# Performance work log

Hardware: AMD Instinct MI355X
Metric: run time of the kernel (lower is better)

The kernel has to match this reference:

```python
import jax, jax.numpy as jnp
import numpy as np

E = 65536          # number of edges (cell pairs)
D = 256            # hidden_dim
P = 8              # n_lr_pairs


def setup_inputs() -> dict:
    key = jax.random.key(0)
    k1, k2, k3, k4, k5, k6, k7 = jax.random.split(key, 7)
    scale = 1.0 / np.sqrt(D)
    z_src = jax.random.normal(k1, (E, D), dtype=jnp.float32)
    z_dst = jax.random.normal(k2, (E, D), dtype=jnp.float32)
    lr_pair_idx = jax.random.randint(k3, (E,), 0, P, dtype=jnp.int64)
    # Per-LR-pair Linear(D, D): y = x @ W.T + b  (torch convention, W: [out, in])
    W_lr = jax.random.normal(k4, (P, D, D), dtype=jnp.float32) * scale
    b_lr = jax.random.normal(k5, (P, D), dtype=jnp.float32) * scale
    # nn.Bilinear(D, D, 1): weight [1, D, D], bias [1]
    W_bil = jax.random.normal(k6, (1, D, D), dtype=jnp.float32) * scale
    b_bil = jax.random.normal(k7, (1,), dtype=jnp.float32) * scale
    return {"z_src": z_src, "z_dst": z_dst, "W_lr": W_lr, "b_lr": b_lr,
            "W_bil": W_bil, "b_bil": b_bil, "lr_pair_idx": lr_pair_idx}


def _forward(z_src, z_dst, W_lr, b_lr, W_bil, b_bil, lr_pair_idx):
    # Per-LR-pair linear projection of z_src (MoE-style routing).
    # Fixed small loop over P experts; each iteration is a dense GEMM over
    # all E edges, masked to the edges routed to that pair. All idx values
    # lie in [0, P), so the zeros-init in the original is fully overwritten.
    z_proj = jnp.zeros_like(z_src)
    for p in range(P):
        mask = (lr_pair_idx == p)[:, None]                      # [E, 1]
        y_p = z_src @ W_lr[p].T + b_lr[p]                       # [E, D]
        z_proj = jnp.where(mask, y_p, z_proj)
    # Bilinear scoring: score_e = z_proj_e @ W_bil[0] @ z_dst_e + b_bil
    t = z_proj @ W_bil[0]                                       # [E, D]
    scores = jnp.sum(t * z_dst, axis=-1, keepdims=True) + b_bil  # [E, 1]
    return scores


def reference(z_src, z_dst, W_lr, b_lr, W_bil, b_bil, lr_pair_idx):
    return _forward(z_src, z_dst, W_lr, b_lr, W_bil, b_bil, lr_pair_idx)
```

## Files before the change

### kernel.cpp

```cpp
#include <hip/hip_runtime.h>
#include <hip/hip_bf16.h>
#include <cstddef>

#define NE 65536
#define ND 256
#define NP 8
#define RBLK 64
#define EPB (NE / RBLK)
#define TR 32
#define MAXT 2056

typedef short bf16x8 __attribute__((ext_vector_type(8)));
typedef float f32x4  __attribute__((ext_vector_type(4)));

__device__ __forceinline__ unsigned short f2bf(float f) {
  unsigned int u = __float_as_uint(f);
  u += 0x7FFFu + ((u >> 16) & 1u);
  return (unsigned short)(u >> 16);
}
__device__ __forceinline__ float bf2f(unsigned short h) {
  return __uint_as_float(((unsigned int)h) << 16);
}
__device__ __forceinline__ int load_idx(const void* idxraw, int is32, int e) {
  return is32 ? ((const int*)idxraw)[e] : (int)((const long long*)idxraw)[e];
}
__device__ __forceinline__ int sniff_is32(const void* idxraw, int* lflag, int bsel) {
  int tid = threadIdx.x;
  if (tid == 0) *lflag = 0;
  __syncthreads();
  const unsigned int* w = (const unsigned int*)idxraw;
  unsigned int val = w[((bsel & 63) * 256 + tid) * 2 + 1];
  if (__any(val != 0) && (tid & 63) == 0) atomicOr(lflag, 1);
  __syncthreads();
  return *lflag;
}

__global__ __launch_bounds__(256) void k_pre0(const float* __restrict__ Wbil,
                                              const float* __restrict__ blr,
                                              const void* __restrict__ idxraw,
                                              unsigned short* __restrict__ WbT,
                                              float* __restrict__ v,
                                              int* __restrict__ counts) {
  int b = blockIdx.x, t = threadIdx.x;
  if (b < 32) {
    int s = b * 256 + t;
    int kt = s >> 10, c = (s >> 6) & 15, l = s & 63;
    int col = c * 16 + (l & 15);
    int k0 = kt * 32 + (l >> 4) * 8;
    union { uint4 u; unsigned short h[8]; } uu;
#pragma unroll
    for (int j = 0; j < 8; ++j)
      uu.h[j] = f2bf(Wbil[(k0 + j) * ND + col]);
    *(uint4*)(WbT + (size_t)s * 8) = uu.u;
  } else if (b < 40) {
    int p = b - 32;
    float s = 0.f;
    for (int k = 0; k < ND; ++k)
      s = fmaf(blr[p * ND + k], Wbil[k * ND + t], s);
    v[p * ND + t] = s;
  } else {
    __shared__ int h[NP];
    __shared__ int lflag;
    int hb = b - 40;
    int is32 = sniff_is32(idxraw, &lflag, hb);
    if (t < NP) h[t] = 0;
    __syncthreads();
    int base = hb * EPB;
#pragma unroll
    for (int i = 0; i < EPB / 256; ++i) {
      int p = load_idx(idxraw, is32, base + t + i * 256);
      atomicAdd(&h[p], 1);
    }
    __syncthreads();
    if (t < NP) counts[hb * NP + t] = h[t];
  }
}

__global__ __launch_bounds__(64) void k_scan(const int* __restrict__ counts,
                                             int* __restrict__ hdr,
                                             int* __restrict__ bases) {
  __shared__ int cnt[NP];
  __shared__ int off[NP + 1];
  int q = threadIdx.x;
  if (q < NP) {
    int s = 0;
    for (int b = 0; b < RBLK; ++b) s += counts[b * NP + q];
    cnt[q] = s;
  }
  __syncthreads();
  if (q == 0) {
    int o = 0, tt = 0;
    for (int p = 0; p < NP; ++p) {
      off[p] = o; hdr[p] = o; hdr[9 + p] = tt;
      o += cnt[p];
      tt += (cnt[p] + TR - 1) / TR;
    }
    off[NP] = o; hdr[NP] = o; hdr[9 + NP] = tt;
  }
  __syncthreads();
  if (q < NP) {
    int run = off[q];
    for (int b = 0; b < RBLK; ++b) {
      bases[b * NP + q] = run;
      run += counts[b * NP + q];
    }
  }
}

__global__ __launch_bounds__(256) void k_sc2(const void* __restrict__ idxraw,
                                             const int* __restrict__ bases,
                                             int* __restrict__ perm,
                                             const float* __restrict__ Wlr,
                                             const unsigned short* __restrict__ WbT,
                                             unsigned short* __restrict__ Cst) {
  __shared__ unsigned short aF[2048 * 8];
  int b = blockIdx.x, tid = threadIdx.x;
  if (b < 64) {
    __shared__ int cur[NP];
    __shared__ int lflag;
    int is32 = sniff_is32(idxraw, &lflag, b);
    if (tid < NP) cur[tid] = bases[b * NP + tid];
    __syncthreads();
    int base = b * EPB;
#pragma unroll
    for (int i = 0; i < EPB / 256; ++i) {
      int e = base + tid + i * 256;
      int p = load_idx(idxraw, is32, e);
      int slot = atomicAdd(&cur[p], 1);
      perm[slot] = e;
    }
    return;
  }
  int blk = b - 64;
  int p = blk >> 2;
  int i0 = (blk & 3) * 64;
  const float* Wp = Wlr + (size_t)p * ND * ND;
#pragma unroll
  for (int it = 0; it < 8; ++it) {
    int s = tid + it * 256;
    int kt = s >> 8, r = (s >> 6) & 3, l = s & 63;
    int i = r * 16 + (l & 15);
    int k0 = kt * 32 + (l >> 4) * 8;
    union { uint4 u; unsigned short h[8]; } uu;
#pragma unroll
    for (int j = 0; j < 8; ++j)
      uu.h[j] = f2bf(Wp[(size_t)(k0 + j) * ND + i0 + i]);
    *(uint4*)(aF + (size_t)s * 8) = uu.u;
  }
  __syncthreads();
  int w = tid >> 6, l = tid & 63;
  f32x4 zero = {0.f, 0.f, 0.f, 0.f};
  f32x4 acc[16];
#pragma unroll
  for (int c = 0; c < 16; ++c) acc[c] = zero;
  for (int kt = 0; kt < 8; ++kt) {
    bf16x8 a = *(const bf16x8*)(aF + (size_t)((kt * 4 + w) * 64 + l) * 8);
#pragma unroll
    for (int c = 0; c < 16; ++c) {
      bf16x8 bb = *(const bf16x8*)(WbT + (size_t)((kt * 16 + c) * 64 + l) * 8);
      acc[c] = __builtin_amdgcn_mfma_f32_16x16x32_bf16(a, bb, acc[c], 0, 0, 0);
    }
  }
  unsigned short* Cp = Cst + (size_t)p * ND * ND;
#pragma unroll
  for (int c = 0; c < 16; ++c) {
#pragma unroll
    for (int q = 0; q < 4; ++q) {
      int i = i0 + w * 16 + ((l >> 4) * 4) + q;
      int j = c * 16 + (l & 15);
      int pos = ((i >> 5) * 16 + (j >> 4)) * 512 + (((i >> 3) & 3) * 16 + (j & 15)) * 8 + (i & 7);
      Cp[pos] = f2bf(acc[c][q]);
    }
  }
}

__global__ __launch_bounds__(512, 6) void k_main(const float* __restrict__ zsrc,
                                                 const float* __restrict__ zdst,
                                                 const int* __restrict__ perm,
                                                 const int* __restrict__ hdr,
                                                 const unsigned short* __restrict__ Cst,
                                                 const float* __restrict__ v,
                                                 const float* __restrict__ bbil,
                                                 float* __restrict__ out) {
  __shared__ unsigned short zs[8192];
  __shared__ unsigned short zd[8192];
  __shared__ float red[8][TR];
  int tid = threadIdx.x;
  int bid = blockIdx.x;
  if (bid >= hdr[9 + NP]) return;
  int p = 0;
#pragma unroll
  for (int q = 1; q < NP; ++q) p += (bid >= hdr[9 + q]) ? 1 : 0;
  int t = bid - hdr[9 + p];
  int cbeg = hdr[p], cend = hdr[p + 1];
  int ebase = cbeg + t * TR;
  int nrow = cend - ebase; if (nrow > TR) nrow = TR;
  int w = tid >> 6, l = tid & 63;

  int e4[4];
#pragma unroll
  for (int i = 0; i < 4; ++i) {
    int r = ebase + w * 4 + i; if (r > cend - 1) r = cend - 1;
    e4[i] = perm[r];
  }
  float4 fs[4], fd[4];
#pragma unroll
  for (int i = 0; i < 4; ++i)
    fs[i] = *(const float4*)(zsrc + (size_t)e4[i] * ND + l * 4);
#pragma unroll
  for (int i = 0; i < 4; ++i)
    fd[i] = *(const float4*)(zdst + (size_t)e4[i] * ND + l * 4);
  int kt0 = l >> 3, q0 = (l >> 1) & 3, par0 = l & 1;
#pragma unroll
  for (int i = 0; i < 4; ++i) {
    int row = w * 4 + i;
    union { unsigned long long u; unsigned short h[4]; } us, ud;
    us.h[0] = f2bf(fs[i].x); us.h[1] = f2bf(fs[i].y);
    us.h[2] = f2bf(fs[i].z); us.h[3] = f2bf(fs[i].w);
    ud.h[0] = f2bf(fd[i].x); ud.h[1] = f2bf(fd[i].y);
    ud.h[2] = f2bf(fd[i].z); ud.h[3] = f2bf(fd[i].w);
    unsigned g = (unsigned)((kt0 * 2 + (row >> 4)) * 64 + (row & 15) + 16 * q0);
    g ^= ((g >> 6) & 7u) << 1;
    *(unsigned long long*)((char*)zs + g * 16 + par0 * 8) = us.u;
    *(unsigned long long*)((char*)zd + ((unsigned)(row * 512 + l * 8) ^ (((unsigned)row & 7u) << 5))) = ud.u;
  }
  __syncthreads();

  const unsigned short* Cp = Cst + (size_t)p * ND * ND;
  f32x4 zero = {0.f, 0.f, 0.f, 0.f};
  f32x4 acc[2][2];
#pragma unroll
  for (int sr = 0; sr < 2; ++sr)
#pragma unroll
    for (int cl = 0; cl < 2; ++cl) acc[sr][cl] = zero;
  int hh = l >> 4, rr = l & 15;
#pragma unroll
  for (int kt = 0; kt < 8; ++kt) {
    bf16x8 a[2];
#pragma unroll
    for (int sr = 0; sr < 2; ++sr) {
      unsigned g = (unsigned)((kt * 2 + sr) * 64 + l);
      g ^= ((g >> 6) & 7u) << 1;
      a[sr] = *(const bf16x8*)((const char*)zs + g * 16);
    }
#pragma unroll
    for (int cl = 0; cl < 2; ++cl) {
      bf16x8 bb = *(const bf16x8*)(Cp + (size_t)((kt * 16 + (w * 2 + cl)) * 64 + l) * 8);
#pragma unroll
      for (int sr = 0; sr < 2; ++sr)
        acc[sr][cl] = __builtin_amdgcn_mfma_f32_16x16x32_bf16(a[sr], bb, acc[sr][cl], 0, 0, 0);
    }
  }

  float vloc[2];
#pragma unroll
  for (int cl = 0; cl < 2; ++cl)
    vloc[cl] = v[p * ND + (w * 2 + cl) * 16 + rr];
#pragma unroll
  for (int sr = 0; sr < 2; ++sr) {
#pragma unroll
    for (int q = 0; q < 4; ++q) {
      int row = sr * 16 + hh * 4 + q;
      unsigned swz = ((unsigned)row & 7u) << 5;
      float sv = 0.f;
#pragma unroll
      for (int cl = 0; cl < 2; ++cl) {
        int col = (w * 2 + cl) * 16 + rr;
        unsigned byte = ((unsigned)(row * 512 + col * 2)) ^ swz;
        sv = fmaf(acc[sr][cl][q] + vloc[cl], bf2f(*(const unsigned short*)((const char*)zd + byte)), sv);
      }
      sv += __shfl_xor(sv, 1, 64);
      sv += __shfl_xor(sv, 2, 64);
      sv += __shfl_xor(sv, 4, 64);
      sv += __shfl_xor(sv, 8, 64);
      if (rr == 0) red[w][row] = sv;
    }
  }
  __syncthreads();
  if (tid < TR && tid < nrow) {
    float sc = bbil[0];
#pragma unroll
    for (int ww = 0; ww < 8; ++ww) sc += red[ww][tid];
    out[perm[ebase + tid]] = sc;
  }
}

extern "C" void kernel_launch(void* const* d_in, const int* in_sizes, int n_in,
                              void* d_out, int out_size, void* d_ws, size_t ws_size,
                              hipStream_t stream) {
  const float* zsrc = (const float*)d_in[0];
  const float* zdst = (const float*)d_in[1];
  const float* Wlr  = (const float*)d_in[2];
  const float* blr  = (const float*)d_in[3];
  const float* Wbil = (const float*)d_in[4];
  const float* bbil = (const float*)d_in[5];
  const void*  idx  = (const void*)d_in[6];
  float* out = (float*)d_out;

  char* ws = (char*)d_ws;
  int* hdr    = (int*)ws;
  int* counts = (int*)(ws + 4096);
  int* bases  = (int*)(ws + 8192);
  int* perm   = (int*)(ws + 16384);
  unsigned short* WbT = (unsigned short*)(ws + 16384 + (size_t)NE * 4);
  float* v = (float*)(ws + 16384 + (size_t)NE * 4 + 131072);
  unsigned short* Cst = (unsigned short*)(ws + 16384 + (size_t)NE * 4 + 131072 + 8192);

  k_pre0<<<104, 256, 0, stream>>>(Wbil, blr, idx, WbT, v, counts);
  k_scan<<<1, 64, 0, stream>>>(counts, hdr, bases);
  k_sc2<<<96, 256, 0, stream>>>(idx, bases, perm, Wlr, WbT, Cst);
  k_main<<<MAXT, 512, 0, stream>>>(zsrc, zdst, perm, hdr, Cst, v, bbil, out);
}
```

Baseline: 75.88 us.

## Stage gathered rows into LDS via direct global_load_lds with fp32 slab

The main kernel now gathers z_src and z_dst rows straight into a swizzled fp32 LDS slab using the global_load_lds builtin, so the data no longer passes through registers. Conversion to bf16 moves to the point where MFMA A-fragments are read. Blocks shrink from 512 to 256 threads, with each wave computing four column tiles instead of two, and edge ids are cached in shared memory. The cost is twice the LDS footprint (64KB fp32 slab), which lowers occupancy, plus conversion work repeated inside the k loop.

```diff
diff --git a/kernel.cpp b/kernel.cpp
--- a/kernel.cpp
+++ b/kernel.cpp
@@ -12,14 +12,13 @@
 
 typedef short bf16x8 __attribute__((ext_vector_type(8)));
 typedef float f32x4  __attribute__((ext_vector_type(4)));
+typedef const __attribute__((address_space(1))) unsigned int* gas_t;
+typedef __attribute__((address_space(3))) unsigned int* las_t;
 
 __device__ __forceinline__ unsigned short f2bf(float f) {
   unsigned int u = __float_as_uint(f);
   u += 0x7FFFu + ((u >> 16) & 1u);
   return (unsigned short)(u >> 16);
-}
-__device__ __forceinline__ float bf2f(unsigned short h) {
-  return __uint_as_float(((unsigned int)h) << 16);
 }
 __device__ __forceinline__ int load_idx(const void* idxraw, int is32, int e) {
   return is32 ? ((const int*)idxraw)[e] : (int)((const long long*)idxraw)[e];
@@ -174,7 +173,7 @@
   }
 }
 
-__global__ __launch_bounds__(512, 6) void k_main(const float* __restrict__ zsrc,
+__global__ __launch_bounds__(256, 2) void k_main(const float* __restrict__ zsrc,
                                                  const float* __restrict__ zdst,
                                                  const int* __restrict__ perm,
                                                  const int* __restrict__ hdr,
@@ -182,9 +181,9 @@
                                                  const float* __restrict__ v,
                                                  const float* __restrict__ bbil,
                                                  float* __restrict__ out) {
-  __shared__ unsigned short zs[8192];
-  __shared__ unsigned short zd[8192];
-  __shared__ float red[8][TR];
+  __shared__ float slab[64][256];
+  __shared__ float red[4][TR];
+  __shared__ int eids[TR];
   int tid = threadIdx.x;
   int bid = blockIdx.x;
   if (bid >= hdr[9 + NP]) return;
@@ -195,79 +194,73 @@
   int cbeg = hdr[p], cend = hdr[p + 1];
   int ebase = cbeg + t * TR;
   int nrow = cend - ebase; if (nrow > TR) nrow = TR;
+  if (tid < TR) {
+    int r = ebase + tid; if (r > cend - 1) r = cend - 1;
+    eids[tid] = perm[r];
+  }
+  __syncthreads();
   int w = tid >> 6, l = tid & 63;
 
-  int e4[4];
-#pragma unroll
-  for (int i = 0; i < 4; ++i) {
-    int r = ebase + w * 4 + i; if (r > cend - 1) r = cend - 1;
-    e4[i] = perm[r];
-  }
-  float4 fs[4], fd[4];
-#pragma unroll
-  for (int i = 0; i < 4; ++i)
-    fs[i] = *(const float4*)(zsrc + (size_t)e4[i] * ND + l * 4);
-#pragma unroll
-  for (int i = 0; i < 4; ++i)
-    fd[i] = *(const float4*)(zdst + (size_t)e4[i] * ND + l * 4);
-  int kt0 = l >> 3, q0 = (l >> 1) & 3, par0 = l & 1;
-#pragma unroll
-  for (int i = 0; i < 4; ++i) {
-    int row = w * 4 + i;
-    union { unsigned long long u; unsigned short h[4]; } us, ud;
-    us.h[0] = f2bf(fs[i].x); us.h[1] = f2bf(fs[i].y);
-    us.h[2] = f2bf(fs[i].z); us.h[3] = f2bf(fs[i].w);
-    ud.h[0] = f2bf(fd[i].x); ud.h[1] = f2bf(fd[i].y);
-    ud.h[2] = f2bf(fd[i].z); ud.h[3] = f2bf(fd[i].w);
-    unsigned g = (unsigned)((kt0 * 2 + (row >> 4)) * 64 + (row & 15) + 16 * q0);
-    g ^= ((g >> 6) & 7u) << 1;
-    *(unsigned long long*)((char*)zs + g * 16 + par0 * 8) = us.u;
-    *(unsigned long long*)((char*)zd + ((unsigned)(row * 512 + l * 8) ^ (((unsigned)row & 7u) << 5))) = ud.u;
+#pragma unroll
+  for (int i = 0; i < 16; ++i) {
+    int r = w * 16 + i;
+    int er = r & 31;
+    const float* g = ((r < 32) ? zsrc : zdst) + (size_t)eids[er] * ND;
+    unsigned off = (unsigned)((l ^ (r & 7)) << 2);
+    __builtin_amdgcn_global_load_lds((gas_t)(const void*)(g + off),
+                                     (las_t)(void*)&slab[r][0], 16, 0, 0);
   }
   __syncthreads();
 
   const unsigned short* Cp = Cst + (size_t)p * ND * ND;
   f32x4 zero = {0.f, 0.f, 0.f, 0.f};
-  f32x4 acc[2][2];
+  f32x4 acc[2][4];
 #pragma unroll
   for (int sr = 0; sr < 2; ++sr)
 #pragma unroll
-    for (int cl = 0; cl < 2; ++cl) acc[sr][cl] = zero;
-  int hh = l >> 4, rr = l & 15;
+    for (int cl = 0; cl < 4; ++cl) acc[sr][cl] = zero;
+  int hi = l >> 4, rr = l & 15;
+  unsigned sxr = (unsigned)(rr & 7);
 #pragma unroll
   for (int kt = 0; kt < 8; ++kt) {
     bf16x8 a[2];
 #pragma unroll
     for (int sr = 0; sr < 2; ++sr) {
-      unsigned g = (unsigned)((kt * 2 + sr) * 64 + l);
-      g ^= ((g >> 6) & 7u) << 1;
-      a[sr] = *(const bf16x8*)((const char*)zs + g * 16);
-    }
-#pragma unroll
-    for (int cl = 0; cl < 2; ++cl) {
-      bf16x8 bb = *(const bf16x8*)(Cp + (size_t)((kt * 16 + (w * 2 + cl)) * 64 + l) * 8);
+      const char* rowb = (const char*)&slab[sr * 16 + rr][0];
+      unsigned g0 = (unsigned)(kt * 8 + hi * 2);
+      float4 f0 = *(const float4*)(rowb + ((g0 ^ sxr) << 4));
+      float4 f1 = *(const float4*)(rowb + (((g0 + 1) ^ sxr) << 4));
+      union { bf16x8 vv; unsigned short h[8]; } ua;
+      ua.h[0] = f2bf(f0.x); ua.h[1] = f2bf(f0.y); ua.h[2] = f2bf(f0.z); ua.h[3] = f2bf(f0.w);
+      ua.h[4] = f2bf(f1.x); ua.h[5] = f2bf(f1.y); ua.h[6] = f2bf(f1.z); ua.h[7] = f2bf(f1.w);
+      a[sr] = ua.vv;
+    }
+#pragma unroll
+    for (int cl = 0; cl < 4; ++cl) {
+      bf16x8 bb = *(const bf16x8*)(Cp + (size_t)((kt * 16 + (w * 4 + cl)) * 64 + l) * 8);
 #pragma unroll
       for (int sr = 0; sr < 2; ++sr)
         acc[sr][cl] = __builtin_amdgcn_mfma_f32_16x16x32_bf16(a[sr], bb, acc[sr][cl], 0, 0, 0);
     }
   }
 
-  float vloc[2];
-#pragma unroll
-  for (int cl = 0; cl < 2; ++cl)
-    vloc[cl] = v[p * ND + (w * 2 + cl) * 16 + rr];
+  float vloc[4];
+#pragma unroll
+  for (int cl = 0; cl < 4; ++cl)
+    vloc[cl] = v[p * ND + (w * 4 + cl) * 16 + rr];
 #pragma unroll
   for (int sr = 0; sr < 2; ++sr) {
 #pragma unroll
     for (int q = 0; q < 4; ++q) {
-      int row = sr * 16 + hh * 4 + q;
-      unsigned swz = ((unsigned)row & 7u) << 5;
+      int row = sr * 16 + hi * 4 + q;
+      const char* zdb = (const char*)&slab[32 + row][0];
+      unsigned sw = (unsigned)(row & 7);
       float sv = 0.f;
 #pragma unroll
-      for (int cl = 0; cl < 2; ++cl) {
-        int col = (w * 2 + cl) * 16 + rr;
-        unsigned byte = ((unsigned)(row * 512 + col * 2)) ^ swz;
-        sv = fmaf(acc[sr][cl][q] + vloc[cl], bf2f(*(const unsigned short*)((const char*)zd + byte)), sv);
+      for (int cl = 0; cl < 4; ++cl) {
+        int col = (w * 4 + cl) * 16 + rr;
+        float zv = *(const float*)(zdb + ((((unsigned)(col >> 2) ^ sw) << 4) | ((unsigned)(col & 3) << 2)));
+        sv = fmaf(acc[sr][cl][q] + vloc[cl], zv, sv);
       }
       sv += __shfl_xor(sv, 1, 64);
       sv += __shfl_xor(sv, 2, 64);
@@ -280,8 +273,8 @@
   if (tid < TR && tid < nrow) {
     float sc = bbil[0];
 #pragma unroll
-    for (int ww = 0; ww < 8; ++ww) sc += red[ww][tid];
-    out[perm[ebase + tid]] = sc;
+    for (int ww = 0; ww < 4; ++ww) sc += red[ww][tid];
+    out[eids[tid]] = sc;
   }
 }
 
@@ -309,5 +302,5 @@
   k_pre0<<<104, 256, 0, stream>>>(Wbil, blr, idx, WbT, v, counts);
   k_scan<<<1, 64, 0, stream>>>(counts, hdr, bases);
   k_sc2<<<96, 256, 0, stream>>>(idx, bases, perm, Wlr, WbT, Cst);
-  k_main<<<MAXT, 512, 0, stream>>>(zsrc, zdst, perm, hdr, Cst, v, bbil, out);
-}
+  k_main<<<MAXT, 256, 0, stream>>>(zsrc, zdst, perm, hdr, Cst, v, bbil, out);
+}
```

Result: slower. 88.92 us (+17.2%).
